# Kernel optimization log

Hardware: AMD Instinct MI355X
Metric: run time of the kernel (lower is better)

The kernel has to match this reference:

```python
import jax, jax.numpy as jnp
import numpy as np

D = 1024

def setup_inputs() -> dict:
    key = jax.random.key(0)
    ks = jax.random.split(key, 7)
    s = 1.0 / np.sqrt(D)  # torch Linear default init scale (uniform bound)
    x = jax.random.normal(ks[0], (4, 2048, D), dtype=jnp.float32)
    Wq = jax.random.uniform(ks[1], (D, D), jnp.float32, -s, s)
    Wk = jax.random.uniform(ks[2], (D, D), jnp.float32, -s, s)
    Wv = jax.random.uniform(ks[3], (D, D), jnp.float32, -s, s)
    bq = jax.random.uniform(ks[4], (D,), jnp.float32, -s, s)
    bk = jax.random.uniform(ks[5], (D,), jnp.float32, -s, s)
    bv = jax.random.uniform(ks[6], (D,), jnp.float32, -s, s)
    return {"x": x, "Wq": Wq, "bq": bq, "Wk": Wk, "bk": bk, "Wv": Wv, "bv": bv}

def reference(x, Wq, bq, Wk, bk, Wv, bv):
    # Linear layers: y = x @ W^T + b (weights stored torch-style [out, in])
    Q = jnp.einsum('bsd,ed->bse', x, Wq) + bq
    K = jnp.einsum('bsd,ed->bse', x, Wk) + bk
    V = jnp.einsum('bsd,ed->bse', x, Wv) + bv
    scale = jnp.sqrt(jnp.asarray(Q.shape[-1], Q.dtype))
    scores = jnp.einsum('bqd,bkd->bqk', Q, K) / scale  # [B, S, S]
    probs = jax.nn.softmax(scores, axis=-1)
    return jnp.einsum('bqk,bkd->bqd', probs, V)
```

## Files before the change

kernel.cpp:

```cpp
#include <hip/hip_runtime.h>


typedef __bf16 bf16x8 __attribute__((ext_vector_type(8)));
typedef float f32x4 __attribute__((ext_vector_type(4)));
typedef unsigned short u16;

__device__ __forceinline__ u16 f2b(float f) {
  union { float f; unsigned u; } a; a.f = f;
  unsigned r = a.u + 0x7fffu + ((a.u >> 16) & 1u);
  return (u16)(r >> 16);
}

__global__ __launch_bounds__(256) void cast_all_kernel(const float* __restrict__ x,
                                                       const float* __restrict__ Wq,
                                                       const float* __restrict__ Wk,
                                                       const float* __restrict__ Wv,
                                                       u16* __restrict__ xb,
                                                       u16* __restrict__ Wb) {
  int b = blockIdx.x;
  if (b < 8192) {
    const int i = b * 256 + threadIdx.x;
    float4 v = reinterpret_cast<const float4*>(x)[i];
    reinterpret_cast<ushort4*>(xb)[i] =
        make_ushort4(f2b(v.x), f2b(v.y), f2b(v.z), f2b(v.w));
  } else {
    b -= 8192;
    const int w = b >> 10;
    const float* src = (w == 0) ? Wq : (w == 1) ? Wk : Wv;
    const int i = (b & 1023) * 256 + threadIdx.x;
    float4 v = reinterpret_cast<const float4*>(src)[i];
    reinterpret_cast<ushort4*>(Wb + (size_t)w * 1048576)[i] =
        make_ushort4(f2b(v.x), f2b(v.y), f2b(v.z), f2b(v.w));
  }
}

template <int GEOM, int NT>
__device__ __forceinline__ void core8(const char* __restrict__ Ab,
                                      const char* __restrict__ Bb, int lda, int ldb,
                                      char* smem, f32x4* acc) {
  constexpr int LDSBUF = GEOM ? 49152 : 65536;
  constexpr int BOFF = GEOM ? 16384 : 32768;
  constexpr int AHALF = GEOM ? 8192 : 16384;
  const int tid = threadIdx.x;
  const int wave = tid >> 6, lane = tid & 63;
  const int wr = wave >> 2, wc = wave & 3;
  const int fr = lane & 15, fg = lane >> 4;
  const int rd = (fr * 64 + fg * 16) ^ (((fr >> 3) & 1) << 5);
  const int li = (lane * 16) ^ ((lane >> 5) << 5);
  const int sr = li >> 6, sc2 = li & 63;

  auto STAGE = [&](int kt, int p) {
    const int isB = p & 1, s = p >> 1;
    char* lds = smem + (kt & 1) * LDSBUF + (isB ? BOFF + s * 16384 : s * AHALF);
    const char* gb = isB ? Bb : Ab;
    const int ldx = isB ? ldb : lda;
    const int colOff = kt * 128 + s * 64 + sc2;
    __builtin_amdgcn_global_load_lds(
        (const __attribute__((address_space(1))) void*)(gb + (size_t)(wave * 16 + sr) * ldx + colOff),
        (__attribute__((address_space(3))) void*)(lds + wave * 1024), 16, 0, 0);
    if (isB || GEOM == 0)
      __builtin_amdgcn_global_load_lds(
          (const __attribute__((address_space(1))) void*)(gb + (size_t)((8 + wave) * 16 + sr) * ldx + colOff),
          (__attribute__((address_space(3))) void*)(lds + 8192 + wave * 1024), 16, 0, 0);
  };

#pragma unroll
  for (int p = 0; p < 4; ++p) STAGE(0, p);
  STAGE(1, 0);
  STAGE(1, 1);
  if constexpr (GEOM == 0) asm volatile("s_waitcnt vmcnt(8)" ::: "memory");
  else asm volatile("s_waitcnt vmcnt(6)" ::: "memory");
  __builtin_amdgcn_s_barrier();
  __builtin_amdgcn_sched_barrier(0);

  bf16x8 keep[4];
  for (int kt = 0; kt < NT; ++kt) {
    const char* bufA = smem + (kt & 1) * LDSBUF;
    const char* bufB = bufA + BOFF;
#pragma unroll
    for (int p = 0; p < 4; ++p) {
      const int s = p >> 1, j = p & 1;
      if constexpr (GEOM == 0) {
        bf16x8 afr[4];
        if (j == 0)
#pragma unroll
          for (int n = 0; n < 4; ++n)
            keep[n] = *reinterpret_cast<const bf16x8*>(bufB + s * 16384 + (wc * 4 + n) * 1024 + rd);
#pragma unroll
        for (int m = 0; m < 4; ++m)
          afr[m] = *reinterpret_cast<const bf16x8*>(bufA + s * 16384 + (wr * 8 + j * 4 + m) * 1024 + rd);
        if (p < 2) { if (kt + 1 < NT) STAGE(kt + 1, p + 2); }
        else       { if (kt + 2 < NT) STAGE(kt + 2, p - 2); }
        __builtin_amdgcn_s_barrier();
        __builtin_amdgcn_sched_barrier(0);
        __builtin_amdgcn_s_setprio(1);
#pragma unroll
        for (int m = 0; m < 4; ++m)
#pragma unroll
          for (int n = 0; n < 4; ++n)
            acc[(j * 4 + m) * 4 + n] = __builtin_amdgcn_mfma_f32_16x16x32_bf16(
                afr[m], keep[n], acc[(j * 4 + m) * 4 + n], 0, 0, 0);
        __builtin_amdgcn_s_setprio(0);
      } else {
        bf16x8 bfr[2];
        if (j == 0)
#pragma unroll
          for (int m = 0; m < 4; ++m)
            keep[m] = *reinterpret_cast<const bf16x8*>(bufA + s * AHALF + (wr * 4 + m) * 1024 + rd);
#pragma unroll
        for (int nn = 0; nn < 2; ++nn)
          bfr[nn] = *reinterpret_cast<const bf16x8*>(bufB + s * 16384 + (wc * 4 + j * 2 + nn) * 1024 + rd);
        if (p < 2) { if (kt + 1 < NT) STAGE(kt + 1, p + 2); }
        else       { if (kt + 2 < NT) STAGE(kt + 2, p - 2); }
        __builtin_amdgcn_s_barrier();
        __builtin_amdgcn_sched_barrier(0);
        __builtin_amdgcn_s_setprio(1);
#pragma unroll
        for (int m = 0; m < 4; ++m)
#pragma unroll
          for (int nn = 0; nn < 2; ++nn)
            acc[m * 4 + j * 2 + nn] = __builtin_amdgcn_mfma_f32_16x16x32_bf16(
                keep[m], bfr[nn], acc[m * 4 + j * 2 + nn], 0, 0, 0);
        __builtin_amdgcn_s_setprio(0);
      }
      if (p == 1) {
        if (kt < NT - 1) {
          if constexpr (GEOM == 0) asm volatile("s_waitcnt vmcnt(8)" ::: "memory");
          else asm volatile("s_waitcnt vmcnt(6)" ::: "memory");
        } else {
          asm volatile("s_waitcnt vmcnt(0)" ::: "memory");
        }
      } else if (p == 3) {
        if (kt < NT - 2) {
          if constexpr (GEOM == 0) asm volatile("s_waitcnt vmcnt(8)" ::: "memory");
          else asm volatile("s_waitcnt vmcnt(6)" ::: "memory");
        } else if (kt == NT - 2) {
          if constexpr (GEOM == 0) asm volatile("s_waitcnt vmcnt(4)" ::: "memory");
          else asm volatile("s_waitcnt vmcnt(3)" ::: "memory");
        }
      }
      __builtin_amdgcn_s_barrier();
      __builtin_amdgcn_sched_barrier(0);
    }
  }
}

__global__ __launch_bounds__(512, 2) void proj8_kernel(
    const u16* __restrict__ A, const u16* __restrict__ Bm,
    const float* __restrict__ bq, const float* __restrict__ bk,
    const float* __restrict__ bvv, u16* __restrict__ QK, u16* __restrict__ Vt) {
  extern __shared__ char smem[];
  const int tileM = blockIdx.x * 128, tileN = blockIdx.y * 256;
  f32x4 acc[16] = {};
  core8<1, 16>((const char*)A + (size_t)tileM * 2048,
               (const char*)Bm + (size_t)tileN * 2048, 2048, 2048, smem, acc);
  const int tid = threadIdx.x;
  const int wave = tid >> 6, lane = tid & 63;
  const int wr = wave >> 2, wc = wave & 3, fr = lane & 15, fg = lane >> 4;
  const int w = blockIdx.y >> 2;
  const float* bias = (w == 0) ? bq : (w == 1) ? bk : bvv;
  if (w < 2) {
    u16* O = QK + (size_t)w * 8388608;
#pragma unroll
    for (int mi = 0; mi < 4; ++mi) {
      const int r0 = tileM + wr * 64 + mi * 16 + fg * 4;
#pragma unroll
      for (int n = 0; n < 4; ++n) {
        const int cw = (tileN + wc * 64 + n * 16 + fr) & 1023;
        const float bi = bias[cw];
#pragma unroll
        for (int jj = 0; jj < 4; ++jj)
          O[(size_t)(r0 + jj) * 1024 + cw] = f2b(acc[mi * 4 + n][jj] + bi);
      }
    }
  } else {
#pragma unroll
    for (int mi = 0; mi < 4; ++mi) {
      const int r0 = tileM + wr * 64 + mi * 16 + fg * 4;
      const int b = r0 >> 11, s0 = r0 & 2047;
#pragma unroll
      for (int n = 0; n < 4; ++n) {
        const int cw = (tileN + wc * 64 + n * 16 + fr) & 1023;
        const float bi = bias[cw];
        ushort4 u = make_ushort4(f2b(acc[mi * 4 + n][0] + bi), f2b(acc[mi * 4 + n][1] + bi),
                                 f2b(acc[mi * 4 + n][2] + bi), f2b(acc[mi * 4 + n][3] + bi));
        *reinterpret_cast<ushort4*>(&Vt[(size_t)b * 2097152 + (size_t)cw * 2048 + s0]) = u;
      }
    }
  }
}

__global__ __launch_bounds__(512, 2) void sc8_kernel(const u16* __restrict__ Qb,
                                                     const u16* __restrict__ Kb,
                                                     u16* __restrict__ P,
                                                     float* __restrict__ rowpart) {
  extern __shared__ char smem[];
  const int z = blockIdx.z;
  const int tileM = blockIdx.x * 256, tileN = blockIdx.y * 256;
  f32x4 acc[32] = {};
  core8<0, 16>((const char*)Qb + (size_t)z * 4194304 + (size_t)tileM * 2048,
               (const char*)Kb + (size_t)z * 4194304 + (size_t)tileN * 2048, 2048, 2048,
               smem, acc);
  const int tid = threadIdx.x;
  const int wave = tid >> 6, lane = tid & 63;
  const int wr = wave >> 2, wc = wave & 3, fr = lane & 15, fg = lane >> 4;
  float* rs = (float*)smem;
  u16* Po = P + (size_t)z * 4194304 + (size_t)tileM * 2048 + tileN;
#pragma unroll
  for (int mi = 0; mi < 8; ++mi) {
#pragma unroll
    for (int jj = 0; jj < 4; ++jj) {
      const int rl = wr * 128 + mi * 16 + fg * 4 + jj;
      float part = 0.f;
#pragma unroll
      for (int n = 0; n < 4; ++n) {
        float e = __expf(acc[mi * 4 + n][jj] * 0.03125f);
        part += e;
        Po[(size_t)rl * 2048 + wc * 64 + n * 16 + fr] = f2b(e);
      }
      part += __shfl_xor(part, 1);
      part += __shfl_xor(part, 2);
      part += __shfl_xor(part, 4);
      part += __shfl_xor(part, 8);
      if (fr == 0) rs[wc * 256 + rl] = part;
    }
  }
  __syncthreads();
  if (tid < 256) {
    float s = rs[tid] + rs[256 + tid] + rs[512 + tid] + rs[768 + tid];
    rowpart[(size_t)blockIdx.y * 8192 + z * 2048 + tileM + tid] = s;
  }
}

__global__ __launch_bounds__(512, 2) void pv8_kernel(const u16* __restrict__ P,
                                                     const u16* __restrict__ Vt,
                                                     const float* __restrict__ rowpart,
                                                     float* __restrict__ out) {
  extern __shared__ char smem[];
  const int z = blockIdx.z;
  const int tileM = blockIdx.x * 128, tileN = blockIdx.y * 256;
  float* rinv = (float*)(smem + 98304);
  const int tid = threadIdx.x;
  if (tid < 128) {
    float s = 0.f;
#pragma unroll
    for (int t = 0; t < 8; ++t) s += rowpart[t * 8192 + z * 2048 + tileM + tid];
    rinv[tid] = 1.0f / s;
  }
  f32x4 acc[16] = {};
  core8<1, 32>((const char*)P + (size_t)z * 8388608 + (size_t)tileM * 4096,
               (const char*)Vt + (size_t)z * 4194304 + (size_t)tileN * 4096, 4096, 4096,
               smem, acc);
  const int wave = tid >> 6, lane = tid & 63;
  const int wr = wave >> 2, wc = wave & 3, fr = lane & 15, fg = lane >> 4;
  float* O = out + (size_t)z * 2097152;
#pragma unroll
  for (int mi = 0; mi < 4; ++mi) {
#pragma unroll
    for (int jj = 0; jj < 4; ++jj) {
      const int r = wr * 64 + mi * 16 + fg * 4 + jj;
      const float inv = rinv[r];
#pragma unroll
      for (int n = 0; n < 4; ++n)
        O[(size_t)(tileM + r) * 1024 + tileN + wc * 64 + n * 16 + fr] =
            acc[mi * 4 + n][jj] * inv;
    }
  }
}

extern "C" void kernel_launch(void* const* d_in, const int* in_sizes, int n_in,
                              void* d_out, int out_size, void* d_ws, size_t ws_size,
                              hipStream_t stream) {
  if (ws_size < ((size_t)72 << 20)) return;
  const float* x = (const float*)d_in[0];
  const float* Wq = (const float*)d_in[1];
  const float* bq = (const float*)d_in[2];
  const float* Wk = (const float*)d_in[3];
  const float* bk = (const float*)d_in[4];
  const float* Wv = (const float*)d_in[5];
  const float* bv = (const float*)d_in[6];
  char* ws = (char*)d_ws;
  u16* xb = (u16*)(ws);
  u16* Pb = (u16*)(ws);
  u16* Qb = (u16*)(ws + ((size_t)16 << 20));
  u16* Kb = (u16*)(ws + ((size_t)32 << 20));
  u16* Vt = (u16*)(ws + ((size_t)48 << 20));
  u16* Wb = (u16*)(ws + ((size_t)64 << 20));
  float* rowpart = (float*)(ws + ((size_t)70 << 20));
  float* out = (float*)d_out;

  (void)hipFuncSetAttribute((const void*)proj8_kernel,
                            hipFuncAttributeMaxDynamicSharedMemorySize, 98304);
  (void)hipFuncSetAttribute((const void*)sc8_kernel,
                            hipFuncAttributeMaxDynamicSharedMemorySize, 131072);
  (void)hipFuncSetAttribute((const void*)pv8_kernel,
                            hipFuncAttributeMaxDynamicSharedMemorySize, 98816);

  cast_all_kernel<<<11264, 256, 0, stream>>>(x, Wq, Wk, Wv, xb, Wb);

  proj8_kernel<<<dim3(64, 12), 512, 98304, stream>>>(xb, Wb, bq, bk, bv, Qb, Vt);

  sc8_kernel<<<dim3(8, 8, 4), 512, 131072, stream>>>(Qb, Kb, Pb, rowpart);
  pv8_kernel<<<dim3(16, 4, 4), 512, 98816, stream>>>(Pb, Vt, rowpart, out);
}
```

Measured before the change: 155.7 us.

## Make projection blocks loop over three N tiles with continuous pipelined loads

The projection kernel now launches a third as many blocks along N. Each block walks three consecutive 256-wide output tiles in one software-pipelined loop of 48 k-steps, with the epilogue run every 16 steps. This keeps the double-buffered global-to-LDS prefetch running across tile boundaries, so the pipeline no longer fills and drains per tile. The cost is fewer blocks (256 instead of 768), which lowers parallelism and may leave CUs underused or load-imbalanced.

```diff
diff --git a/kernel.cpp b/kernel.cpp
--- a/kernel.cpp
+++ b/kernel.cpp
@@ -150,42 +150,123 @@
     const float* __restrict__ bq, const float* __restrict__ bk,
     const float* __restrict__ bvv, u16* __restrict__ QK, u16* __restrict__ Vt) {
   extern __shared__ char smem[];
-  const int tileM = blockIdx.x * 128, tileN = blockIdx.y * 256;
-  f32x4 acc[16] = {};
-  core8<1, 16>((const char*)A + (size_t)tileM * 2048,
-               (const char*)Bm + (size_t)tileN * 2048, 2048, 2048, smem, acc);
+  constexpr int FT = 48;
   const int tid = threadIdx.x;
   const int wave = tid >> 6, lane = tid & 63;
-  const int wr = wave >> 2, wc = wave & 3, fr = lane & 15, fg = lane >> 4;
-  const int w = blockIdx.y >> 2;
-  const float* bias = (w == 0) ? bq : (w == 1) ? bk : bvv;
-  if (w < 2) {
-    u16* O = QK + (size_t)w * 8388608;
-#pragma unroll
-    for (int mi = 0; mi < 4; ++mi) {
-      const int r0 = tileM + wr * 64 + mi * 16 + fg * 4;
-#pragma unroll
-      for (int n = 0; n < 4; ++n) {
-        const int cw = (tileN + wc * 64 + n * 16 + fr) & 1023;
-        const float bi = bias[cw];
-#pragma unroll
-        for (int jj = 0; jj < 4; ++jj)
-          O[(size_t)(r0 + jj) * 1024 + cw] = f2b(acc[mi * 4 + n][jj] + bi);
-      }
-    }
-  } else {
-#pragma unroll
-    for (int mi = 0; mi < 4; ++mi) {
-      const int r0 = tileM + wr * 64 + mi * 16 + fg * 4;
-      const int b = r0 >> 11, s0 = r0 & 2047;
-#pragma unroll
-      for (int n = 0; n < 4; ++n) {
-        const int cw = (tileN + wc * 64 + n * 16 + fr) & 1023;
-        const float bi = bias[cw];
-        ushort4 u = make_ushort4(f2b(acc[mi * 4 + n][0] + bi), f2b(acc[mi * 4 + n][1] + bi),
-                                 f2b(acc[mi * 4 + n][2] + bi), f2b(acc[mi * 4 + n][3] + bi));
-        *reinterpret_cast<ushort4*>(&Vt[(size_t)b * 2097152 + (size_t)cw * 2048 + s0]) = u;
-      }
+  const int wr = wave >> 2, wc = wave & 3;
+  const int fr = lane & 15, fg = lane >> 4;
+  const int rd = (fr * 64 + fg * 16) ^ (((fr >> 3) & 1) << 5);
+  const int li = (lane * 16) ^ ((lane >> 5) << 5);
+  const int sr = li >> 6, sc2 = li & 63;
+  const int tileM = blockIdx.x * 128;
+  const int byc = blockIdx.y;
+  const char* Ab = (const char*)A + (size_t)tileM * 2048;
+  const char* Bbase = (const char*)Bm + (size_t)byc * 3 * 524288;
+
+  auto STAGE = [&](int ft, int p) {
+    if (ft >= FT) return;
+    const int t = ft >> 4, kt = ft & 15;
+    const int isB = p & 1, s = p >> 1;
+    char* lds = smem + (ft & 1) * 49152 + (isB ? 16384 + s * 16384 : s * 8192);
+    const int colOff = kt * 128 + s * 64 + sc2;
+    if (!isB) {
+      __builtin_amdgcn_global_load_lds(
+          (const __attribute__((address_space(1))) void*)(Ab + (size_t)(wave * 16 + sr) * 2048 + colOff),
+          (__attribute__((address_space(3))) void*)(lds + wave * 1024), 16, 0, 0);
+    } else {
+      const char* Bb = Bbase + (size_t)t * 524288;
+      __builtin_amdgcn_global_load_lds(
+          (const __attribute__((address_space(1))) void*)(Bb + (size_t)(wave * 16 + sr) * 2048 + colOff),
+          (__attribute__((address_space(3))) void*)(lds + wave * 1024), 16, 0, 0);
+      __builtin_amdgcn_global_load_lds(
+          (const __attribute__((address_space(1))) void*)(Bb + (size_t)((8 + wave) * 16 + sr) * 2048 + colOff),
+          (__attribute__((address_space(3))) void*)(lds + 8192 + wave * 1024), 16, 0, 0);
+    }
+  };
+
+#pragma unroll
+  for (int p = 0; p < 4; ++p) STAGE(0, p);
+  STAGE(1, 0);
+  STAGE(1, 1);
+  asm volatile("s_waitcnt vmcnt(6)" ::: "memory");
+  __builtin_amdgcn_s_barrier();
+  __builtin_amdgcn_sched_barrier(0);
+
+  f32x4 acc[16] = {};
+  bf16x8 keep[4];
+
+  for (int ft = 0; ft < FT; ++ft) {
+    const char* bufA = smem + (ft & 1) * 49152;
+    const char* bufB = bufA + 16384;
+#pragma unroll
+    for (int p = 0; p < 4; ++p) {
+      const int s = p >> 1, j = p & 1;
+      bf16x8 bfr[2];
+      if (j == 0)
+#pragma unroll
+        for (int m = 0; m < 4; ++m)
+          keep[m] = *reinterpret_cast<const bf16x8*>(bufA + s * 8192 + (wr * 4 + m) * 1024 + rd);
+#pragma unroll
+      for (int nn = 0; nn < 2; ++nn)
+        bfr[nn] = *reinterpret_cast<const bf16x8*>(bufB + s * 16384 + (wc * 4 + j * 2 + nn) * 1024 + rd);
+      if (p < 2) STAGE(ft + 1, p + 2);
+      else STAGE(ft + 2, p - 2);
+      __builtin_amdgcn_s_barrier();
+      __builtin_amdgcn_sched_barrier(0);
+      __builtin_amdgcn_s_setprio(1);
+#pragma unroll
+      for (int m = 0; m < 4; ++m)
+#pragma unroll
+        for (int nn = 0; nn < 2; ++nn)
+          acc[m * 4 + j * 2 + nn] = __builtin_amdgcn_mfma_f32_16x16x32_bf16(
+              keep[m], bfr[nn], acc[m * 4 + j * 2 + nn], 0, 0, 0);
+      __builtin_amdgcn_s_setprio(0);
+      if (p == 1) {
+        if (ft < FT - 1) asm volatile("s_waitcnt vmcnt(6)" ::: "memory");
+        else asm volatile("s_waitcnt vmcnt(0)" ::: "memory");
+      } else if (p == 3) {
+        if (ft < FT - 2) asm volatile("s_waitcnt vmcnt(6)" ::: "memory");
+        else if (ft == FT - 2) asm volatile("s_waitcnt vmcnt(3)" ::: "memory");
+      }
+      __builtin_amdgcn_s_barrier();
+      __builtin_amdgcn_sched_barrier(0);
+    }
+    if ((ft & 15) == 15) {
+      const int by = byc * 3 + (ft >> 4);
+      const int tileN = by * 256;
+      const int w = by >> 2;
+      const float* bias = (w == 0) ? bq : (w == 1) ? bk : bvv;
+      if (w < 2) {
+        u16* O = QK + (size_t)w * 8388608;
+#pragma unroll
+        for (int mi = 0; mi < 4; ++mi) {
+          const int r0 = tileM + wr * 64 + mi * 16 + fg * 4;
+#pragma unroll
+          for (int n = 0; n < 4; ++n) {
+            const int cw = (tileN + wc * 64 + n * 16 + fr) & 1023;
+            const float bi = bias[cw];
+#pragma unroll
+            for (int jj = 0; jj < 4; ++jj)
+              O[(size_t)(r0 + jj) * 1024 + cw] = f2b(acc[mi * 4 + n][jj] + bi);
+          }
+        }
+      } else {
+#pragma unroll
+        for (int mi = 0; mi < 4; ++mi) {
+          const int r0 = tileM + wr * 64 + mi * 16 + fg * 4;
+          const int b = r0 >> 11, s0 = r0 & 2047;
+#pragma unroll
+          for (int n = 0; n < 4; ++n) {
+            const int cw = (tileN + wc * 64 + n * 16 + fr) & 1023;
+            const float bi = bias[cw];
+            ushort4 u = make_ushort4(f2b(acc[mi * 4 + n][0] + bi), f2b(acc[mi * 4 + n][1] + bi),
+                                     f2b(acc[mi * 4 + n][2] + bi), f2b(acc[mi * 4 + n][3] + bi));
+            *reinterpret_cast<ushort4*>(&Vt[(size_t)b * 2097152 + (size_t)cw * 2048 + s0]) = u;
+          }
+        }
+      }
+#pragma unroll
+      for (int i = 0; i < 16; ++i) acc[i] = f32x4{};
     }
   }
 }
@@ -298,7 +379,7 @@
 
   cast_all_kernel<<<11264, 256, 0, stream>>>(x, Wq, Wk, Wv, xb, Wb);
 
-  proj8_kernel<<<dim3(64, 12), 512, 98304, stream>>>(xb, Wb, bq, bk, bv, Qb, Vt);
+  proj8_kernel<<<dim3(64, 4), 512, 98304, stream>>>(xb, Wb, bq, bk, bv, Qb, Vt);
 
   sc8_kernel<<<dim3(8, 8, 4), 512, 131072, stream>>>(Qb, Kb, Pb, rowpart);
   pv8_kernel<<<dim3(16, 4, 4), 512, 98816, stream>>>(Pb, Vt, rowpart, out);
```

Result: no change. 157.3 us (+1.0%).

## Simplify GEMM core pipeline to two phases per K-tile with combined A/B staging

Applied to the files above, without the earlier changes.

Replaces the four-phase per-K-tile schedule (alternating A and B half loads, keeping fragments across phases, prefetching two tiles ahead) with a two-phase loop. Each phase loads all A and B fragments for one K-half, stages the matching half of the next tile, and issues every MFMA for that half. This reduces barriers and waitcnt bookkeeping per tile, at the cost of a shallower prefetch distance (one tile instead of partly two) and more fragment registers live at once. A sched_barrier is also added in pv8 before the core so the row-inverse computation is not reordered into it.

```diff
diff --git a/kernel.cpp b/kernel.cpp
--- a/kernel.cpp
+++ b/kernel.cpp
@@ -35,12 +35,13 @@
 }
 
 template <int GEOM, int NT>
-__device__ __forceinline__ void core8(const char* __restrict__ Ab,
+__device__ __forceinline__ void core2(const char* __restrict__ Ab,
                                       const char* __restrict__ Bb, int lda, int ldb,
                                       char* smem, f32x4* acc) {
   constexpr int LDSBUF = GEOM ? 49152 : 65536;
   constexpr int BOFF = GEOM ? 16384 : 32768;
   constexpr int AHALF = GEOM ? 8192 : 16384;
+  constexpr int NA = GEOM ? 4 : 8;
   const int tid = threadIdx.x;
   const int wave = tid >> 6, lane = tid & 63;
   const int wr = wave >> 2, wc = wave & 3;
@@ -49,95 +50,61 @@
   const int li = (lane * 16) ^ ((lane >> 5) << 5);
   const int sr = li >> 6, sc2 = li & 63;
 
-  auto STAGE = [&](int kt, int p) {
-    const int isB = p & 1, s = p >> 1;
-    char* lds = smem + (kt & 1) * LDSBUF + (isB ? BOFF + s * 16384 : s * AHALF);
-    const char* gb = isB ? Bb : Ab;
-    const int ldx = isB ? ldb : lda;
+  auto STAGE = [&](int kt, int s) {
+    char* base = smem + (kt & 1) * LDSBUF;
     const int colOff = kt * 128 + s * 64 + sc2;
+    char* ldsA = base + s * AHALF;
     __builtin_amdgcn_global_load_lds(
-        (const __attribute__((address_space(1))) void*)(gb + (size_t)(wave * 16 + sr) * ldx + colOff),
-        (__attribute__((address_space(3))) void*)(lds + wave * 1024), 16, 0, 0);
-    if (isB || GEOM == 0)
+        (const __attribute__((address_space(1))) void*)(Ab + (size_t)(wave * 16 + sr) * lda + colOff),
+        (__attribute__((address_space(3))) void*)(ldsA + wave * 1024), 16, 0, 0);
+    if constexpr (GEOM == 0)
       __builtin_amdgcn_global_load_lds(
-          (const __attribute__((address_space(1))) void*)(gb + (size_t)((8 + wave) * 16 + sr) * ldx + colOff),
-          (__attribute__((address_space(3))) void*)(lds + 8192 + wave * 1024), 16, 0, 0);
+          (const __attribute__((address_space(1))) void*)(Ab + (size_t)((8 + wave) * 16 + sr) * lda + colOff),
+          (__attribute__((address_space(3))) void*)(ldsA + 8192 + wave * 1024), 16, 0, 0);
+    char* ldsB = base + BOFF + s * 16384;
+    __builtin_amdgcn_global_load_lds(
+        (const __attribute__((address_space(1))) void*)(Bb + (size_t)(wave * 16 + sr) * ldb + colOff),
+        (__attribute__((address_space(3))) void*)(ldsB + wave * 1024), 16, 0, 0);
+    __builtin_amdgcn_global_load_lds(
+        (const __attribute__((address_space(1))) void*)(Bb + (size_t)((8 + wave) * 16 + sr) * ldb + colOff),
+        (__attribute__((address_space(3))) void*)(ldsB + 8192 + wave * 1024), 16, 0, 0);
   };
 
-#pragma unroll
-  for (int p = 0; p < 4; ++p) STAGE(0, p);
-  STAGE(1, 0);
-  STAGE(1, 1);
-  if constexpr (GEOM == 0) asm volatile("s_waitcnt vmcnt(8)" ::: "memory");
-  else asm volatile("s_waitcnt vmcnt(6)" ::: "memory");
+  STAGE(0, 0);
+  STAGE(0, 1);
+  if constexpr (GEOM == 0) asm volatile("s_waitcnt vmcnt(4)" ::: "memory");
+  else asm volatile("s_waitcnt vmcnt(3)" ::: "memory");
   __builtin_amdgcn_s_barrier();
   __builtin_amdgcn_sched_barrier(0);
 
-  bf16x8 keep[4];
   for (int kt = 0; kt < NT; ++kt) {
     const char* bufA = smem + (kt & 1) * LDSBUF;
     const char* bufB = bufA + BOFF;
 #pragma unroll
-    for (int p = 0; p < 4; ++p) {
-      const int s = p >> 1, j = p & 1;
-      if constexpr (GEOM == 0) {
-        bf16x8 afr[4];
-        if (j == 0)
-#pragma unroll
-          for (int n = 0; n < 4; ++n)
-            keep[n] = *reinterpret_cast<const bf16x8*>(bufB + s * 16384 + (wc * 4 + n) * 1024 + rd);
-#pragma unroll
-        for (int m = 0; m < 4; ++m)
-          afr[m] = *reinterpret_cast<const bf16x8*>(bufA + s * 16384 + (wr * 8 + j * 4 + m) * 1024 + rd);
-        if (p < 2) { if (kt + 1 < NT) STAGE(kt + 1, p + 2); }
-        else       { if (kt + 2 < NT) STAGE(kt + 2, p - 2); }
-        __builtin_amdgcn_s_barrier();
-        __builtin_amdgcn_sched_barrier(0);
-        __builtin_amdgcn_s_setprio(1);
-#pragma unroll
-        for (int m = 0; m < 4; ++m)
-#pragma unroll
-          for (int n = 0; n < 4; ++n)
-            acc[(j * 4 + m) * 4 + n] = __builtin_amdgcn_mfma_f32_16x16x32_bf16(
-                afr[m], keep[n], acc[(j * 4 + m) * 4 + n], 0, 0, 0);
-        __builtin_amdgcn_s_setprio(0);
-      } else {
-        bf16x8 bfr[2];
-        if (j == 0)
-#pragma unroll
-          for (int m = 0; m < 4; ++m)
-            keep[m] = *reinterpret_cast<const bf16x8*>(bufA + s * AHALF + (wr * 4 + m) * 1024 + rd);
-#pragma unroll
-        for (int nn = 0; nn < 2; ++nn)
-          bfr[nn] = *reinterpret_cast<const bf16x8*>(bufB + s * 16384 + (wc * 4 + j * 2 + nn) * 1024 + rd);
-        if (p < 2) { if (kt + 1 < NT) STAGE(kt + 1, p + 2); }
-        else       { if (kt + 2 < NT) STAGE(kt + 2, p - 2); }
-        __builtin_amdgcn_s_barrier();
-        __builtin_amdgcn_sched_barrier(0);
-        __builtin_amdgcn_s_setprio(1);
-#pragma unroll
-        for (int m = 0; m < 4; ++m)
-#pragma unroll
-          for (int nn = 0; nn < 2; ++nn)
-            acc[m * 4 + j * 2 + nn] = __builtin_amdgcn_mfma_f32_16x16x32_bf16(
-                keep[m], bfr[nn], acc[m * 4 + j * 2 + nn], 0, 0, 0);
-        __builtin_amdgcn_s_setprio(0);
-      }
-      if (p == 1) {
-        if (kt < NT - 1) {
-          if constexpr (GEOM == 0) asm volatile("s_waitcnt vmcnt(8)" ::: "memory");
-          else asm volatile("s_waitcnt vmcnt(6)" ::: "memory");
-        } else {
-          asm volatile("s_waitcnt vmcnt(0)" ::: "memory");
-        }
-      } else if (p == 3) {
-        if (kt < NT - 2) {
-          if constexpr (GEOM == 0) asm volatile("s_waitcnt vmcnt(8)" ::: "memory");
-          else asm volatile("s_waitcnt vmcnt(6)" ::: "memory");
-        } else if (kt == NT - 2) {
-          if constexpr (GEOM == 0) asm volatile("s_waitcnt vmcnt(4)" ::: "memory");
-          else asm volatile("s_waitcnt vmcnt(3)" ::: "memory");
-        }
+    for (int s = 0; s < 2; ++s) {
+      bf16x8 afr[NA], bfr[4];
+#pragma unroll
+      for (int m = 0; m < NA; ++m)
+        afr[m] = *reinterpret_cast<const bf16x8*>(bufA + s * AHALF + (wr * NA + m) * 1024 + rd);
+#pragma unroll
+      for (int n = 0; n < 4; ++n)
+        bfr[n] = *reinterpret_cast<const bf16x8*>(bufB + s * 16384 + (wc * 4 + n) * 1024 + rd);
+      if (kt + 1 < NT) STAGE(kt + 1, s);
+      __builtin_amdgcn_s_barrier();
+      __builtin_amdgcn_sched_barrier(0);
+      __builtin_amdgcn_s_setprio(1);
+#pragma unroll
+      for (int m = 0; m < NA; ++m)
+#pragma unroll
+        for (int n = 0; n < 4; ++n)
+          acc[m * 4 + n] = __builtin_amdgcn_mfma_f32_16x16x32_bf16(
+              afr[m], bfr[n], acc[m * 4 + n], 0, 0, 0);
+      __builtin_amdgcn_s_setprio(0);
+      if (kt < NT - 1) {
+        if constexpr (GEOM == 0) asm volatile("s_waitcnt vmcnt(4)" ::: "memory");
+        else asm volatile("s_waitcnt vmcnt(3)" ::: "memory");
+      } else if (s == 0) {
+        asm volatile("s_waitcnt vmcnt(0)" ::: "memory");
       }
       __builtin_amdgcn_s_barrier();
       __builtin_amdgcn_sched_barrier(0);
@@ -152,7 +119,7 @@
   extern __shared__ char smem[];
   const int tileM = blockIdx.x * 128, tileN = blockIdx.y * 256;
   f32x4 acc[16] = {};
-  core8<1, 16>((const char*)A + (size_t)tileM * 2048,
+  core2<1, 16>((const char*)A + (size_t)tileM * 2048,
                (const char*)Bm + (size_t)tileN * 2048, 2048, 2048, smem, acc);
   const int tid = threadIdx.x;
   const int wave = tid >> 6, lane = tid & 63;
@@ -198,7 +165,7 @@
   const int z = blockIdx.z;
   const int tileM = blockIdx.x * 256, tileN = blockIdx.y * 256;
   f32x4 acc[32] = {};
-  core8<0, 16>((const char*)Qb + (size_t)z * 4194304 + (size_t)tileM * 2048,
+  core2<0, 16>((const char*)Qb + (size_t)z * 4194304 + (size_t)tileM * 2048,
                (const char*)Kb + (size_t)z * 4194304 + (size_t)tileN * 2048, 2048, 2048,
                smem, acc);
   const int tid = threadIdx.x;
@@ -247,8 +214,9 @@
     for (int t = 0; t < 8; ++t) s += rowpart[t * 8192 + z * 2048 + tileM + tid];
     rinv[tid] = 1.0f / s;
   }
+  __builtin_amdgcn_sched_barrier(0);
   f32x4 acc[16] = {};
-  core8<1, 32>((const char*)P + (size_t)z * 8388608 + (size_t)tileM * 4096,
+  core2<1, 32>((const char*)P + (size_t)z * 8388608 + (size_t)tileM * 4096,
                (const char*)Vt + (size_t)z * 4194304 + (size_t)tileN * 4096, 4096, 4096,
                smem, acc);
   const int wave = tid >> 6, lane = tid & 63;
```

Result: no change. 155.5 us (-0.1%).
